# Performance work log

Hardware: AMD Instinct MI355X
Metric: run time of the kernel (lower is better)

Reference implementation:

```python
import jax, jax.numpy as jnp
import numpy as np

SAMPLE_RATE = 0.1
BINS = int(256 * SAMPLE_RATE)  # 25
KSIZE = 7
EPS = 1e-6


def _pascal_kernel_2d(ksize):
    # kornia get_pascal_kernel_2d(ksize, norm=True): outer product of binomial row, sum=1
    row = np.array([1.0, 6.0, 15.0, 20.0, 15.0, 6.0, 1.0], dtype=np.float32)
    row = row / row.sum()
    k2d = np.outer(row, row)
    return jnp.asarray(k2d, dtype=jnp.float32)


def _blur_pool2d(x, ksize=KSIZE):
    # kornia.filters.blur_pool2d: depthwise conv with pascal kernel, stride 2, zero pad ksize//2
    C = x.shape[1]
    k = jnp.broadcast_to(_pascal_kernel_2d(ksize).astype(x.dtype), (C, 1, ksize, ksize))
    pad = ksize // 2
    return jax.lax.conv_general_dilated(
        x, k, window_strides=(2, 2), padding=((pad, pad), (pad, pad)),
        feature_group_count=C, dimension_numbers=("NCHW", "OIHW", "NCHW"))


def _per_channel_hist(x, bins):
    # torch.histc(v, bins, 0, 1) per (b, c) plane: values outside [0,1] ignored,
    # value == 1 falls in last bin. Fused via one flat scatter-add.
    B, C, H, W = x.shape
    v = x.reshape(B * C, H * W)
    idx = jnp.clip(jnp.floor(v * bins).astype(jnp.int32), 0, bins - 1)
    valid = ((v >= 0.0) & (v <= 1.0)).astype(x.dtype)
    flat_idx = (jnp.arange(B * C, dtype=jnp.int32)[:, None] * bins + idx).reshape(-1)
    hist = jnp.zeros(B * C * bins, dtype=x.dtype).at[flat_idx].add(valid.reshape(-1))
    return hist.reshape(B, C, bins)


def setup_inputs() -> dict:
    key = jax.random.key(0)
    kx, ky = jax.random.split(key)
    B, C, H, W = 32, 3, 512, 512
    x = jax.random.uniform(kx, (B, C, H, W), dtype=jnp.float32)
    y = jax.random.uniform(ky, (B, C, H, W), dtype=jnp.float32)
    return {"x": x, "y": y}


def reference(x, y):
    hw = x.shape[-2] * x.shape[-1]  # original H*W (as in source)
    xb = _blur_pool2d(x)
    yb = _blur_pool2d(y)
    xh = _per_channel_hist(xb, BINS) / hw  # [B, C, BINS]
    yh = _per_channel_hist(yb, BINS) / hw
    # nn.CosineSimilarity(dim=0, eps=1e-6) applied per (b, c) vector pair
    dot = jnp.sum(xh * yh, axis=-1)
    nx = jnp.maximum(jnp.linalg.norm(xh, axis=-1), EPS)
    ny = jnp.maximum(jnp.linalg.norm(yh, axis=-1), EPS)
    cos = dot / (nx * ny)  # [B, C]
    return jnp.mean(cos)
```

## Files before the change

kernel.cpp:

```cpp
#include <hip/hip_runtime.h>

#define BINS 25
#define H 512
#define W 512
#define NPLANES 96
#define TOX 32
#define TOY 16
#define NBX 8
#define NBY 16
#define NBLK (NBX*NBY)
#define TROWS 37
#define RP 72
#define NV4 (TROWS*18)
#define VP 36
#define NSH 16

__device__ __forceinline__ void async_load16(const float* g, float* lds_wave_base) {
    __builtin_amdgcn_global_load_lds(
        (const __attribute__((address_space(1))) void*)g,
        (__attribute__((address_space(3))) void*)lds_wave_base,
        16, 0, 0);
}

__global__ __launch_bounds__(256) void blur_hist(
        const float* __restrict__ x, const float* __restrict__ y,
        unsigned int* __restrict__ partial) {
    const int z = blockIdx.z;
    const float* src = (z < NPLANES) ? x + (size_t)z * H * W
                                     : y + (size_t)(z - NPLANES) * H * W;

    __shared__ __align__(16) float raw[TROWS * RP];
    __shared__ __align__(16) float ve[TOY * VP];
    __shared__ __align__(16) float vo[TOY * VP];
    __shared__ __align__(16) unsigned int sh[NSH * BINS];

    const int tid = threadIdx.x;
    const int base_x = 2 * (blockIdx.x * TOX) - 4;
    const int base_y = 2 * (blockIdx.y * TOY) - 3;

    if (tid < 100) {
        float4 z4 = make_float4(0.f, 0.f, 0.f, 0.f);
        *(float4*)((float*)sh + 4 * tid) = z4;
    }

    const bool interior = (base_x >= 0) && (base_x + RP <= W) &&
                          (base_y >= 0) && (base_y + TROWS <= H);
    if (interior) {
        #pragma unroll
        for (int k = 0; k < 3; k++) {
            int v = 256 * k + tid;
            if (v < NV4) {
                int r = v / 18;
                int c = v - r * 18;
                const float* g = src + (size_t)(base_y + r) * W + base_x + 4 * c;
                float* dst = raw + (size_t)(256 * k + (tid & ~63)) * 4;
                async_load16(g, dst);
            }
        }
    } else {
        const bool xfull = (base_x >= 0) && (base_x + RP <= W);
        for (int v = tid; v < NV4; v += 256) {
            int r  = v / 18;
            int c4 = v - r * 18;
            int gy = base_y + r;
            int gx = base_x + 4 * c4;
            float4 val = make_float4(0.f, 0.f, 0.f, 0.f);
            if (gy >= 0 && gy < H) {
                if (xfull) {
                    val = *(const float4*)(src + (size_t)gy * W + gx);
                } else {
                    const size_t rb = (size_t)gy * W;
                    if (gx + 0 >= 0 && gx + 0 < W) val.x = src[rb + gx + 0];
                    if (gx + 1 >= 0 && gx + 1 < W) val.y = src[rb + gx + 1];
                    if (gx + 2 >= 0 && gx + 2 < W) val.z = src[rb + gx + 2];
                    if (gx + 3 >= 0 && gx + 3 < W) val.w = src[rb + gx + 3];
                }
            }
            *(float4*)(raw + r * RP + 4 * c4) = val;
        }
    }
    __syncthreads();

    const float w0 = 1.f/64.f, w1 = 6.f/64.f, w2 = 15.f/64.f, w3 = 20.f/64.f;

    for (int v = tid; v < TOY * 18; v += 256) {
        int ly = v / 18;
        int q  = v - ly * 18;
        const float* p = raw + (2 * ly) * RP + 4 * q;
        float4 a0 = *(const float4*)(p + 0 * RP);
        float4 a1 = *(const float4*)(p + 1 * RP);
        float4 a2 = *(const float4*)(p + 2 * RP);
        float4 a3 = *(const float4*)(p + 3 * RP);
        float4 a4 = *(const float4*)(p + 4 * RP);
        float4 a5 = *(const float4*)(p + 5 * RP);
        float4 a6 = *(const float4*)(p + 6 * RP);
        float s0 = w0*(a0.x+a6.x) + w1*(a1.x+a5.x) + w2*(a2.x+a4.x) + w3*a3.x;
        float s1 = w0*(a0.y+a6.y) + w1*(a1.y+a5.y) + w2*(a2.y+a4.y) + w3*a3.y;
        float s2 = w0*(a0.z+a6.z) + w1*(a1.z+a5.z) + w2*(a2.z+a4.z) + w3*a3.z;
        float s3 = w0*(a0.w+a6.w) + w1*(a1.w+a5.w) + w2*(a2.w+a4.w) + w3*a3.w;
        *(float2*)(ve + ly * VP + 2 * q) = make_float2(s0, s2);
        *(float2*)(vo + ly * VP + 2 * q) = make_float2(s1, s3);
    }
    __syncthreads();

    if (tid < 128) {
        const int ly = tid >> 3;
        const int qq = tid & 7;
        const float* ob = vo + ly * VP + 4 * qq;
        const float* eb = ve + ly * VP + 4 * qq;
        float4 A = *(const float4*)(ob);
        float4 B = *(const float4*)(ob + 4);
        float4 C = *(const float4*)(eb);
        float4 D = *(const float4*)(eb + 4);
        float oa[8] = {A.x, A.y, A.z, A.w, B.x, B.y, B.z, B.w};
        float ea[8] = {C.x, C.y, C.z, C.w, D.x, D.y, D.z, D.w};
        unsigned int* wh = sh + (tid & (NSH - 1)) * BINS;
        #pragma unroll
        for (int j = 0; j < 4; j++) {
            float s = w0*(oa[j] + oa[j+3]) + w2*(oa[j+1] + oa[j+2])
                    + w1*(ea[j+1] + ea[j+3]) + w3*ea[j+2];
            int b = min((int)(s * 25.f), BINS - 1);
            atomicAdd(&wh[b], 1u);
        }
    }
    __syncthreads();

    if (tid < BINS) {
        unsigned int s = 0;
        #pragma unroll
        for (int g = 0; g < NSH; g++) s += sh[g * BINS + tid];
        int blk = blockIdx.y * NBX + blockIdx.x;
        partial[((size_t)z * NBLK + blk) * BINS + tid] = s;
    }
}

__global__ __launch_bounds__(256) void reduce_cos(
        const unsigned int* __restrict__ partial, float* __restrict__ out) {
    __shared__ unsigned int sh[2 * BINS];
    const int p = blockIdx.x;
    const int t = threadIdx.x;
    if (t < 2 * BINS) sh[t] = 0u;
    __syncthreads();
    const unsigned int* xp = partial + (size_t)p * NBLK * BINS;
    const unsigned int* yp = partial + (size_t)(NPLANES + p) * NBLK * BINS;
    for (int f = t; f < NBLK * BINS; f += 256) {
        int b = f % BINS;
        atomicAdd(&sh[b], xp[f]);
        atomicAdd(&sh[BINS + b], yp[f]);
    }
    __syncthreads();
    if (t == 0) {
        const float inv_hw = 1.0f / (float)(H * W);
        float dot = 0.f, nx = 0.f, ny = 0.f;
        for (int i = 0; i < BINS; i++) {
            float a = (float)sh[i] * inv_hw;
            float b = (float)sh[BINS + i] * inv_hw;
            dot += a * b;
            nx  += a * a;
            ny  += b * b;
        }
        nx = fmaxf(sqrtf(nx), 1e-6f);
        ny = fmaxf(sqrtf(ny), 1e-6f);
        atomicAdd(out, (dot / (nx * ny)) * (1.0f / (float)NPLANES));
    }
}

extern "C" void kernel_launch(void* const* d_in, const int* in_sizes, int n_in,
                              void* d_out, int out_size, void* d_ws, size_t ws_size,
                              hipStream_t stream) {
    const float* x = (const float*)d_in[0];
    const float* y = (const float*)d_in[1];
    float* out = (float*)d_out;

    unsigned int* partial = (unsigned int*)d_ws;

    hipMemsetAsync(out, 0, sizeof(float), stream);

    dim3 grd(NBX, NBY, 2 * NPLANES);
    blur_hist<<<grd, 256, 0, stream>>>(x, y, partial);

    reduce_cos<<<NPLANES, 256, 0, stream>>>(partial, out);
}
```

Baseline: 229.8 us.

## Make blur-hist blocks persistent over column bands with register-prefetched tiles

Each block now handles a band of 8 vertically consecutive output tiles instead of one tile. It prefetches the next tile's input into registers while the current tile runs the vertical and horizontal blur passes, with one LDS buffer. The grid shrinks from 24576 to 3072 blocks, which cuts per-block setup and histogram flush costs and shrinks the partial array the reduction reads. The async global-to-LDS load path is replaced by register loads, and the 4-row overlap between adjacent tiles is still loaded again rather than reused. Fewer blocks may lower the parallelism available for hiding latency.

```diff
diff --git a/kernel.cpp b/kernel.cpp
--- a/kernel.cpp
+++ b/kernel.cpp
@@ -6,26 +6,23 @@
 #define NPLANES 96
 #define TOX 32
 #define TOY 16
-#define NBX 8
-#define NBY 16
-#define NBLK (NBX*NBY)
 #define TROWS 37
 #define RP 72
 #define NV4 (TROWS*18)
 #define VP 36
 #define NSH 16
-
-__device__ __forceinline__ void async_load16(const float* g, float* lds_wave_base) {
-    __builtin_amdgcn_global_load_lds(
-        (const __attribute__((address_space(1))) void*)g,
-        (__attribute__((address_space(3))) void*)lds_wave_base,
-        16, 0, 0);
-}
+#define TPB 8
+#define NBANDS (2*NPLANES*8*2)
 
 __global__ __launch_bounds__(256) void blur_hist(
         const float* __restrict__ x, const float* __restrict__ y,
         unsigned int* __restrict__ partial) {
-    const int z = blockIdx.z;
+    const int band = blockIdx.x;
+    const int z    = band >> 4;
+    const int r16  = band & 15;
+    const int bx   = r16 >> 1;
+    const int ty0  = (r16 & 1) * TPB;
+
     const float* src = (z < NPLANES) ? x + (size_t)z * H * W
                                      : y + (size_t)(z - NPLANES) * H * W;
 
@@ -35,57 +32,55 @@
     __shared__ __align__(16) unsigned int sh[NSH * BINS];
 
     const int tid = threadIdx.x;
-    const int base_x = 2 * (blockIdx.x * TOX) - 4;
-    const int base_y = 2 * (blockIdx.y * TOY) - 3;
+    const int base_x = 64 * bx - 4;
 
-    if (tid < 100) {
-        float4 z4 = make_float4(0.f, 0.f, 0.f, 0.f);
-        *(float4*)((float*)sh + 4 * tid) = z4;
+    if (tid < 100) *(float4*)((float*)sh + 4 * tid) = make_float4(0.f, 0.f, 0.f, 0.f);
+
+    int rr[3], off[3];
+    bool ld[3];
+    #pragma unroll
+    for (int k = 0; k < 3; k++) {
+        int v = tid + 256 * k;
+        int r = v / 18;
+        int c4 = v - 18 * r;
+        rr[k]  = r;
+        off[k] = r * W + base_x + 4 * c4;
+        bool inr  = (v < NV4);
+        bool xoob = (bx == 0 && c4 == 0) || (bx == 7 && c4 == 17);
+        ld[k] = inr && !xoob;
     }
 
-    const bool interior = (base_x >= 0) && (base_x + RP <= W) &&
-                          (base_y >= 0) && (base_y + TROWS <= H);
-    if (interior) {
+    float4 P[3];
+    auto loadtile = [&](int T) {
+        const ptrdiff_t tb = (ptrdiff_t)(32 * T - 3) * W;
+        const bool ychk = (T == 0) || (T == 15);
         #pragma unroll
         for (int k = 0; k < 3; k++) {
-            int v = 256 * k + tid;
-            if (v < NV4) {
-                int r = v / 18;
-                int c = v - r * 18;
-                const float* g = src + (size_t)(base_y + r) * W + base_x + 4 * c;
-                float* dst = raw + (size_t)(256 * k + (tid & ~63)) * 4;
-                async_load16(g, dst);
-            }
-        }
-    } else {
-        const bool xfull = (base_x >= 0) && (base_x + RP <= W);
-        for (int v = tid; v < NV4; v += 256) {
-            int r  = v / 18;
-            int c4 = v - r * 18;
-            int gy = base_y + r;
-            int gx = base_x + 4 * c4;
-            float4 val = make_float4(0.f, 0.f, 0.f, 0.f);
-            if (gy >= 0 && gy < H) {
-                if (xfull) {
-                    val = *(const float4*)(src + (size_t)gy * W + gx);
+            float4 v4 = make_float4(0.f, 0.f, 0.f, 0.f);
+            if (ld[k]) {
+                if (ychk) {
+                    int gy = 32 * T - 3 + rr[k];
+                    if (gy >= 0 && gy < H) v4 = *(const float4*)(src + tb + off[k]);
                 } else {
-                    const size_t rb = (size_t)gy * W;
-                    if (gx + 0 >= 0 && gx + 0 < W) val.x = src[rb + gx + 0];
-                    if (gx + 1 >= 0 && gx + 1 < W) val.y = src[rb + gx + 1];
-                    if (gx + 2 >= 0 && gx + 2 < W) val.z = src[rb + gx + 2];
-                    if (gx + 3 >= 0 && gx + 3 < W) val.w = src[rb + gx + 3];
+                    v4 = *(const float4*)(src + tb + off[k]);
                 }
             }
-            *(float4*)(raw + r * RP + 4 * c4) = val;
+            P[k] = v4;
         }
-    }
-    __syncthreads();
+    };
+    auto writeraw = [&]() {
+        *(float4*)(raw + 4 * (tid + 0))   = P[0];
+        *(float4*)(raw + 4 * (tid + 256)) = P[1];
+        if (tid < NV4 - 512) *(float4*)(raw + 4 * (tid + 512)) = P[2];
+    };
 
     const float w0 = 1.f/64.f, w1 = 6.f/64.f, w2 = 15.f/64.f, w3 = 20.f/64.f;
 
-    for (int v = tid; v < TOY * 18; v += 256) {
-        int ly = v / 18;
-        int q  = v - ly * 18;
+    const int ly_a = tid / 18, q_a = tid - 18 * ly_a;
+    const int vb = tid + 256;
+    const int ly_b = vb / 18, q_b = vb - 18 * ly_b;
+
+    auto vpass = [&](int ly, int q) {
         const float* p = raw + (2 * ly) * RP + 4 * q;
         float4 a0 = *(const float4*)(p + 0 * RP);
         float4 a1 = *(const float4*)(p + 1 * RP);
@@ -100,61 +95,82 @@
         float s3 = w0*(a0.w+a6.w) + w1*(a1.w+a5.w) + w2*(a2.w+a4.w) + w3*a3.w;
         *(float2*)(ve + ly * VP + 2 * q) = make_float2(s0, s2);
         *(float2*)(vo + ly * VP + 2 * q) = make_float2(s1, s3);
+    };
+    auto stage2 = [&]() {
+        vpass(ly_a, q_a);
+        if (tid < 32) vpass(ly_b, q_b);
+    };
+
+    const int ly3 = tid >> 3;
+    const int qq  = tid & 7;
+    unsigned int* wh = sh + (tid & (NSH - 1)) * BINS;
+    auto stage3 = [&]() {
+        if (tid < 128) {
+            const float* ob = vo + ly3 * VP + 4 * qq;
+            const float* eb = ve + ly3 * VP + 4 * qq;
+            float4 A = *(const float4*)(ob);
+            float4 B = *(const float4*)(ob + 4);
+            float4 C = *(const float4*)(eb);
+            float4 D = *(const float4*)(eb + 4);
+            float oa[8] = {A.x, A.y, A.z, A.w, B.x, B.y, B.z, B.w};
+            float ea[8] = {C.x, C.y, C.z, C.w, D.x, D.y, D.z, D.w};
+            #pragma unroll
+            for (int j = 0; j < 4; j++) {
+                float s = w0*(oa[j] + oa[j+3]) + w2*(oa[j+1] + oa[j+2])
+                        + w1*(ea[j+1] + ea[j+3]) + w3*ea[j+2];
+                int b = min((int)(s * 25.f), BINS - 1);
+                atomicAdd(&wh[b], 1u);
+            }
+        }
+    };
+
+    loadtile(ty0);
+    writeraw();
+    __syncthreads();
+    #pragma unroll 1
+    for (int i = 0; i < TPB - 1; i++) {
+        loadtile(ty0 + i + 1);
+        stage2();
+        __syncthreads();
+        stage3();
+        writeraw();
+        __syncthreads();
     }
+    stage2();
     __syncthreads();
-
-    if (tid < 128) {
-        const int ly = tid >> 3;
-        const int qq = tid & 7;
-        const float* ob = vo + ly * VP + 4 * qq;
-        const float* eb = ve + ly * VP + 4 * qq;
-        float4 A = *(const float4*)(ob);
-        float4 B = *(const float4*)(ob + 4);
-        float4 C = *(const float4*)(eb);
-        float4 D = *(const float4*)(eb + 4);
-        float oa[8] = {A.x, A.y, A.z, A.w, B.x, B.y, B.z, B.w};
-        float ea[8] = {C.x, C.y, C.z, C.w, D.x, D.y, D.z, D.w};
-        unsigned int* wh = sh + (tid & (NSH - 1)) * BINS;
-        #pragma unroll
-        for (int j = 0; j < 4; j++) {
-            float s = w0*(oa[j] + oa[j+3]) + w2*(oa[j+1] + oa[j+2])
-                    + w1*(ea[j+1] + ea[j+3]) + w3*ea[j+2];
-            int b = min((int)(s * 25.f), BINS - 1);
-            atomicAdd(&wh[b], 1u);
-        }
-    }
+    stage3();
     __syncthreads();
 
     if (tid < BINS) {
         unsigned int s = 0;
         #pragma unroll
         for (int g = 0; g < NSH; g++) s += sh[g * BINS + tid];
-        int blk = blockIdx.y * NBX + blockIdx.x;
-        partial[((size_t)z * NBLK + blk) * BINS + tid] = s;
+        partial[band * BINS + tid] = s;
     }
 }
 
-__global__ __launch_bounds__(256) void reduce_cos(
+__global__ __launch_bounds__(64) void reduce_cos(
         const unsigned int* __restrict__ partial, float* __restrict__ out) {
-    __shared__ unsigned int sh[2 * BINS];
+    __shared__ float sa[BINS], sb[BINS];
     const int p = blockIdx.x;
     const int t = threadIdx.x;
-    if (t < 2 * BINS) sh[t] = 0u;
-    __syncthreads();
-    const unsigned int* xp = partial + (size_t)p * NBLK * BINS;
-    const unsigned int* yp = partial + (size_t)(NPLANES + p) * NBLK * BINS;
-    for (int f = t; f < NBLK * BINS; f += 256) {
-        int b = f % BINS;
-        atomicAdd(&sh[b], xp[f]);
-        atomicAdd(&sh[BINS + b], yp[f]);
+    if (t < BINS) {
+        unsigned int a = 0, b = 0;
+        #pragma unroll
+        for (int j = 0; j < 16; j++) {
+            a += partial[((size_t)(p) * 16 + j) * BINS + t];
+            b += partial[((size_t)(NPLANES + p) * 16 + j) * BINS + t];
+        }
+        sa[t] = (float)a;
+        sb[t] = (float)b;
     }
     __syncthreads();
     if (t == 0) {
         const float inv_hw = 1.0f / (float)(H * W);
         float dot = 0.f, nx = 0.f, ny = 0.f;
         for (int i = 0; i < BINS; i++) {
-            float a = (float)sh[i] * inv_hw;
-            float b = (float)sh[BINS + i] * inv_hw;
+            float a = sa[i] * inv_hw;
+            float b = sb[i] * inv_hw;
             dot += a * b;
             nx  += a * a;
             ny  += b * b;
@@ -176,8 +192,6 @@
 
     hipMemsetAsync(out, 0, sizeof(float), stream);
 
-    dim3 grd(NBX, NBY, 2 * NPLANES);
-    blur_hist<<<grd, 256, 0, stream>>>(x, y, partial);
-
-    reduce_cos<<<NPLANES, 256, 0, stream>>>(partial, out);
+    blur_hist<<<NBANDS, 256, 0, stream>>>(x, y, partial);
+    reduce_cos<<<NPLANES, 64, 0, stream>>>(partial, out);
 }
```

Result: slower. 234.6 us (+2.1%).
